# Kernel tuning notes

Measured on AMD Instinct MI355X. Metric: run time of the kernel, lower is better.

The kernel has to match this reference:

```python
import jax, jax.numpy as jnp
import numpy as np

# Graph configuration: G equal-sized graphs of N nodes each.
G, N, E, F = 64, 1024, 1_048_576, 256
RATIO, MULT = 0.5, 1.0
K = max(1, min(int(np.ceil(N * RATIO)), N))  # per-graph top-k = 512


def setup_inputs() -> dict:
    key = jax.random.key(0)
    k1, k2, k3, k4 = jax.random.split(key, 4)
    x = jax.random.normal(k1, (G * N, F), dtype=jnp.float32)
    # Edges constrained within a graph so per-graph pooling is meaningful.
    g = jax.random.randint(k2, (E,), 0, G)
    src = g * N + jax.random.randint(k3, (E,), 0, N)
    dst = g * N + jax.random.randint(k4, (E,), 0, N)
    edge_index = jnp.stack([src, dst]).astype(jnp.int32)  # [2, E]
    batch = jnp.repeat(jnp.arange(G, dtype=jnp.int32), N)  # [G*N]
    return {"x": x, "edge_index": edge_index, "batch": batch}


def reference(x, edge_index, batch):
    num_nodes = x.shape[0]
    # compute_score: out-degree via scatter-add of ones onto edge_index[0]
    degree = jnp.zeros(num_nodes, jnp.float32).at[edge_index[0]].add(1.0)
    score = degree  # min_score is None

    # Per-graph top-k. Graphs are equal-sized (N nodes), contiguous in batch
    # order, so the Python loop over graphs collapses to a batched top_k.
    _, topk_idx = jax.lax.top_k(score.reshape(G, N), K)  # [G, K]
    offsets = (jnp.arange(G, dtype=topk_idx.dtype) * N)[:, None]
    perm = (topk_idx + offsets).reshape(-1)  # [G*K] global node ids

    x_filtered = x[perm] * MULT
    batch_filtered = batch[perm]
    score_filtered = score[perm]

    # filter_edges_manual: keep edges whose both endpoints survive, remap ids.
    node_mask = jnp.zeros(num_nodes, bool).at[perm].set(True)
    edge_mask = node_mask[edge_index[1]] & node_mask[edge_index[0]]  # [E]
    node_map = jnp.full(num_nodes, -1, edge_index.dtype).at[perm].set(
        jnp.arange(perm.shape[0], dtype=edge_index.dtype))
    # Fixed-shape (jit-safe) variant of edge_index[:, edge_mask]: dropped
    # edges are marked -1; edge_mask identifies surviving edges.
    remapped_edge_index = jnp.where(edge_mask[None, :], node_map[edge_index], -1)

    return (x_filtered, remapped_edge_index, batch_filtered, perm,
            score_filtered, edge_mask)
```

## Files before the change

### kernel.cpp

```cpp
#include <hip/hip_runtime.h>


#define NG     64
#define NN     1024
#define NF     256
#define NK     512
#define HBLK   128
#define HWORDS 16384
#define NB2    256
#define EBLK   1024

__global__ void zero_kernel(int* __restrict__ p, int n) {
    int i = blockIdx.x * blockDim.x + threadIdx.x;
    if (i < n) p[i] = 0;
}

__global__ void degree_kernel(const int* __restrict__ ei_src,
                              int* __restrict__ deg, int E) {
    int e = blockIdx.x * blockDim.x + threadIdx.x;
    if (e < E) atomicAdd(&deg[ei_src[e]], 1);
}

__global__ __launch_bounds__(1024) void hist_kernel(
        const int* __restrict__ ei_src, unsigned int* __restrict__ hist_ws,
        int edges_per_blk) {
    __shared__ unsigned int h[HWORDS];
    const int tid = threadIdx.x;
    #pragma unroll
    for (int i = 0; i < HWORDS / 1024; ++i) h[i * 1024 + tid] = 0;
    __syncthreads();

    const int n4 = edges_per_blk >> 2;
    const int4* e4 = (const int4*)ei_src + (size_t)blockIdx.x * n4;
    for (int i = tid; i < n4; i += 1024) {
        const int4 v = e4[i];
        atomicAdd(&h[v.x >> 2], 1u << ((v.x & 3) << 3));
        atomicAdd(&h[v.y >> 2], 1u << ((v.y & 3) << 3));
        atomicAdd(&h[v.z >> 2], 1u << ((v.z & 3) << 3));
        atomicAdd(&h[v.w >> 2], 1u << ((v.w & 3) << 3));
    }
    __syncthreads();

    unsigned int* dst = hist_ws + (size_t)blockIdx.x * HWORDS;
    #pragma unroll
    for (int i = 0; i < HWORDS / 1024; ++i) dst[i * 1024 + tid] = h[i * 1024 + tid];
}

template <bool FUSED>
__global__ __launch_bounds__(1024) void rank_kernel(
        const unsigned int* __restrict__ hist_ws, const int* __restrict__ deg,
        int* __restrict__ node_map, float* __restrict__ out_perm,
        float* __restrict__ out_batch, float* __restrict__ out_score) {
    const int g = blockIdx.x, tid = threadIdx.x;
    const int wave = tid >> 6, lane = tid & 63;

    __shared__ unsigned int psum[4][256];
    __shared__ unsigned short whist[16][NB2];
    __shared__ int suf[NB2];

    ((unsigned int*)whist)[tid] = 0;
    ((unsigned int*)whist)[tid + 1024] = 0;

    int d;
    if (FUSED) {
        const int wl = tid & 255, grp = tid >> 8;
        const unsigned int* p =
            hist_ws + (size_t)(grp * 32) * HWORDS + (g * 256 + wl);
        unsigned int s = 0;
        #pragma unroll 8
        for (int b = 0; b < 32; ++b) s += p[(size_t)b * HWORDS];
        psum[grp][wl] = s;
        __syncthreads();
        const int w = tid >> 2, sh = (tid & 3) << 3;
        d = (int)((psum[0][w] >> sh) & 0xffu) + (int)((psum[1][w] >> sh) & 0xffu)
          + (int)((psum[2][w] >> sh) & 0xffu) + (int)((psum[3][w] >> sh) & 0xffu);
    } else {
        d = deg[g * NN + tid];
        __syncthreads();
    }
    const int b = d < NB2 ? d : (NB2 - 1);

    unsigned long long peers = ~0ull;
    #pragma unroll
    for (int k = 0; k < 8; ++k) {
        const bool bit = (b >> k) & 1;
        const unsigned long long m = __ballot(bit);
        peers &= bit ? m : ~m;
    }
    const unsigned long long lt = (1ull << lane) - 1ull;
    const int intra = __popcll(peers & lt);
    if (intra == 0)
        whist[wave][b] = (unsigned short)__popcll(peers);
    __syncthreads();

    if (tid < NB2) {
        int t = 0;
        #pragma unroll
        for (int w = 0; w < 16; ++w) t += whist[w][tid];
        suf[tid] = t;
    }
    __syncthreads();
    for (int off = 1; off < NB2; off <<= 1) {
        int v = 0;
        if (tid < NB2) v = suf[tid] + ((tid + off < NB2) ? suf[tid + off] : 0);
        __syncthreads();
        if (tid < NB2) suf[tid] = v;
        __syncthreads();
    }

    int cross = 0;
    for (int w = 0; w < 16; ++w) cross += (w < wave) ? whist[w][b] : 0;

    const int cnt_gt = (b < NB2 - 1) ? suf[b + 1] : 0;
    const int rank = cnt_gt + cross + intra;

    const int gid = g * NN + tid;
    const int nm = (rank < NK) ? (g * NK + rank) : -1;
    node_map[gid] = nm;
    if (nm >= 0) {
        out_perm[nm]  = (float)gid;
        out_batch[nm] = (float)g;
        out_score[nm] = (float)d;
    }
}

__global__ void out_kernel(const float* __restrict__ x,
                           const float* __restrict__ out_perm,
                           float* __restrict__ out_x,
                           const int* __restrict__ ei,
                           const int* __restrict__ node_map,
                           float* __restrict__ out_e,
                           float* __restrict__ out_mask, int E) {
    const int bid = blockIdx.x;
    if (bid < EBLK) {
        const int n4 = E >> 2;
        const int i = bid * 256 + threadIdx.x;
        if (i >= n4) return;
        const int4* e4 = (const int4*)ei;
        const int4 s = e4[i];
        const int4 t = e4[n4 + i];
        const int ms0 = node_map[s.x], ms1 = node_map[s.y];
        const int ms2 = node_map[s.z], ms3 = node_map[s.w];
        const int mt0 = node_map[t.x], mt1 = node_map[t.y];
        const int mt2 = node_map[t.z], mt3 = node_map[t.w];
        const bool k0 = (ms0 >= 0) & (mt0 >= 0);
        const bool k1 = (ms1 >= 0) & (mt1 >= 0);
        const bool k2 = (ms2 >= 0) & (mt2 >= 0);
        const bool k3 = (ms3 >= 0) & (mt3 >= 0);
        float4 es, et, mk;
        es.x = k0 ? (float)ms0 : -1.0f;  et.x = k0 ? (float)mt0 : -1.0f;
        es.y = k1 ? (float)ms1 : -1.0f;  et.y = k1 ? (float)mt1 : -1.0f;
        es.z = k2 ? (float)ms2 : -1.0f;  et.z = k2 ? (float)mt2 : -1.0f;
        es.w = k3 ? (float)ms3 : -1.0f;  et.w = k3 ? (float)mt3 : -1.0f;
        mk.x = k0 ? 1.0f : 0.0f;  mk.y = k1 ? 1.0f : 0.0f;
        mk.z = k2 ? 1.0f : 0.0f;  mk.w = k3 ? 1.0f : 0.0f;
        ((float4*)out_e)[i]      = es;
        ((float4*)out_e)[n4 + i] = et;
        ((float4*)out_mask)[i]   = mk;
    } else {
        const int flat = (bid - EBLK) * 256 + threadIdx.x;
        const int row  = flat >> 6;
        const int lane = flat & 63;
        if (row >= NG * NK) return;
        const int src = (int)out_perm[row];
        const float4* xs = (const float4*)(x + (size_t)src * NF);
        float4* xd = (float4*)(out_x + (size_t)row * NF);
        xd[lane] = xs[lane];
    }
}

extern "C" void kernel_launch(void* const* d_in, const int* in_sizes, int n_in,
                              void* d_out, int out_size, void* d_ws, size_t ws_size,
                              hipStream_t stream) {
    (void)n_in; (void)out_size;

    const float* x  = (const float*)d_in[0];
    const int*   ei = (const int*)d_in[1];
    const int E = in_sizes[1] / 2;
    const int num_nodes = in_sizes[2];

    float* out = (float*)d_out;
    size_t off = 0;
    float* out_x     = out + off; off += (size_t)NG * NK * NF;
    float* out_e     = out + off; off += 2 * (size_t)E;
    float* out_batch = out + off; off += (size_t)NG * NK;
    float* out_perm  = out + off; off += (size_t)NG * NK;
    float* out_score = out + off; off += (size_t)NG * NK;
    float* out_mask  = out + off;

    const int gather_blocks = (NG * NK * 64) / 256;
    const size_t hist_bytes = (size_t)HBLK * HWORDS * sizeof(unsigned int);
    const size_t need = hist_bytes + (size_t)num_nodes * sizeof(int);

    if (ws_size >= need) {
        unsigned int* hist_ws = (unsigned int*)d_ws;
        int* node_map = (int*)((char*)d_ws + hist_bytes);

        hist_kernel<<<HBLK, 1024, 0, stream>>>(ei, hist_ws, E / HBLK);
        rank_kernel<true><<<NG, 1024, 0, stream>>>(hist_ws, nullptr, node_map,
                                                   out_perm, out_batch, out_score);
        out_kernel<<<EBLK + gather_blocks, 256, 0, stream>>>(
            x, out_perm, out_x, ei, node_map, out_e, out_mask, E);
    } else {
        int* deg      = (int*)d_ws;
        int* node_map = deg + num_nodes;
        zero_kernel<<<(num_nodes + 255) / 256, 256, 0, stream>>>(deg, num_nodes);
        degree_kernel<<<(E + 255) / 256, 256, 0, stream>>>(ei, deg, E);
        rank_kernel<false><<<NG, 1024, 0, stream>>>(nullptr, deg, node_map,
                                                    out_perm, out_batch, out_score);
        out_kernel<<<EBLK + gather_blocks, 256, 0, stream>>>(
            x, out_perm, out_x, ei, node_map, out_e, out_mask, E);
    }
}
```

Baseline: 37.94 us.

## Split histogram reduction into a wide reduce kernel and double histogram blocks

Doubles the number of per-block edge histogram partials, so the histogram stage can spread over more compute units. Moves the cross-partial summation out of the 64-block rank kernel into a new 256-block reduce kernel that writes packed per-node degrees. The rank kernel then reads one packed word per four nodes. The cost is twice as much partial-histogram traffic written and read, plus one more kernel launch. It still relies on 8-bit packed counts not overflowing.

```diff
diff --git a/kernel.cpp b/kernel.cpp
--- a/kernel.cpp
+++ b/kernel.cpp
@@ -5,7 +5,7 @@
 #define NN     1024
 #define NF     256
 #define NK     512
-#define HBLK   128
+#define HBLK   256
 #define HWORDS 16384
 #define NB2    256
 #define EBLK   1024
@@ -46,37 +46,46 @@
     for (int i = 0; i < HWORDS / 1024; ++i) dst[i * 1024 + tid] = h[i * 1024 + tid];
 }
 
+__global__ __launch_bounds__(256) void reduce_kernel(
+        const unsigned int* __restrict__ hist_ws,
+        unsigned int* __restrict__ packed_deg) {
+    __shared__ unsigned int lsum[4][64];
+    const int t = threadIdx.x;
+    const int q = t >> 6, wl = t & 63;
+    const int w = blockIdx.x * 64 + wl;
+    const unsigned int* p = hist_ws + (size_t)(q * 64) * HWORDS + w;
+    unsigned int s = 0;
+    #pragma unroll 8
+    for (int j = 0; j < 64; ++j) s += p[(size_t)j * HWORDS];
+    lsum[q][wl] = s;
+    __syncthreads();
+    if (t < 64) {
+        packed_deg[blockIdx.x * 64 + t] =
+            lsum[0][t] + lsum[1][t] + lsum[2][t] + lsum[3][t];
+    }
+}
+
 template <bool FUSED>
 __global__ __launch_bounds__(1024) void rank_kernel(
-        const unsigned int* __restrict__ hist_ws, const int* __restrict__ deg,
+        const unsigned int* __restrict__ packed_deg, const int* __restrict__ deg,
         int* __restrict__ node_map, float* __restrict__ out_perm,
         float* __restrict__ out_batch, float* __restrict__ out_score) {
     const int g = blockIdx.x, tid = threadIdx.x;
     const int wave = tid >> 6, lane = tid & 63;
 
-    __shared__ unsigned int psum[4][256];
     __shared__ unsigned short whist[16][NB2];
     __shared__ int suf[NB2];
 
     ((unsigned int*)whist)[tid] = 0;
     ((unsigned int*)whist)[tid + 1024] = 0;
+    __syncthreads();
 
     int d;
     if (FUSED) {
-        const int wl = tid & 255, grp = tid >> 8;
-        const unsigned int* p =
-            hist_ws + (size_t)(grp * 32) * HWORDS + (g * 256 + wl);
-        unsigned int s = 0;
-        #pragma unroll 8
-        for (int b = 0; b < 32; ++b) s += p[(size_t)b * HWORDS];
-        psum[grp][wl] = s;
-        __syncthreads();
-        const int w = tid >> 2, sh = (tid & 3) << 3;
-        d = (int)((psum[0][w] >> sh) & 0xffu) + (int)((psum[1][w] >> sh) & 0xffu)
-          + (int)((psum[2][w] >> sh) & 0xffu) + (int)((psum[3][w] >> sh) & 0xffu);
+        const unsigned int w = packed_deg[g * 256 + (tid >> 2)];
+        d = (int)((w >> ((tid & 3) << 3)) & 0xffu);
     } else {
         d = deg[g * NN + tid];
-        __syncthreads();
     }
     const int b = d < NB2 ? d : (NB2 - 1);
 
@@ -190,14 +199,17 @@
 
     const int gather_blocks = (NG * NK * 64) / 256;
     const size_t hist_bytes = (size_t)HBLK * HWORDS * sizeof(unsigned int);
-    const size_t need = hist_bytes + (size_t)num_nodes * sizeof(int);
+    const size_t deg_bytes  = (size_t)HWORDS * sizeof(unsigned int);
+    const size_t need = hist_bytes + deg_bytes + (size_t)num_nodes * sizeof(int);
 
     if (ws_size >= need) {
-        unsigned int* hist_ws = (unsigned int*)d_ws;
-        int* node_map = (int*)((char*)d_ws + hist_bytes);
+        unsigned int* hist_ws    = (unsigned int*)d_ws;
+        unsigned int* packed_deg = hist_ws + (size_t)HBLK * HWORDS;
+        int* node_map = (int*)(packed_deg + HWORDS);
 
         hist_kernel<<<HBLK, 1024, 0, stream>>>(ei, hist_ws, E / HBLK);
-        rank_kernel<true><<<NG, 1024, 0, stream>>>(hist_ws, nullptr, node_map,
+        reduce_kernel<<<HWORDS / 64, 256, 0, stream>>>(hist_ws, packed_deg);
+        rank_kernel<true><<<NG, 1024, 0, stream>>>(packed_deg, nullptr, node_map,
                                                    out_perm, out_batch, out_score);
         out_kernel<<<EBLK + gather_blocks, 256, 0, stream>>>(
             x, out_perm, out_x, ei, node_map, out_e, out_mask, E);
```

New measurement: 40.87 us. 7.7% more time.

## Fuse histogram, rank and output stages into one persistent kernel with grid barriers

Applied to the files above, without the earlier changes.

Replaces the three-kernel pipeline (histogram, rank, output) with one persistent 256-block kernel that separates stages using software grid barriers built on agent-scope atomics. The degree reduction is split into its own parallel stage that writes packed degrees, so the rank stage only reads a small array. The intent is to remove two kernel launch gaps and use all blocks for the cross-histogram reduction. In exchange, correctness depends on all 256 blocks being co-resident, the barrier spin loop has a timeout that could silently break ordering, a memset is added per call, and only 64 blocks do useful work during the rank stage.

```diff
diff --git a/kernel.cpp b/kernel.cpp
--- a/kernel.cpp
+++ b/kernel.cpp
@@ -5,94 +5,218 @@
 #define NN     1024
 #define NF     256
 #define NK     512
-#define HBLK   128
+#define GRID   256
 #define HWORDS 16384
 #define NB2    256
-#define EBLK   1024
+
+__device__ __forceinline__ void grid_barrier(unsigned int* bar,
+                                             unsigned int target) {
+    __syncthreads();
+    if (threadIdx.x == 0) {
+        __threadfence();
+        const unsigned int old = __hip_atomic_fetch_add(
+            &bar[0], 1u, __ATOMIC_ACQ_REL, __HIP_MEMORY_SCOPE_AGENT);
+        if (old == GRID - 1) {
+            __hip_atomic_store(&bar[0], 0u, __ATOMIC_RELAXED,
+                               __HIP_MEMORY_SCOPE_AGENT);
+            __hip_atomic_store(&bar[1], target, __ATOMIC_RELEASE,
+                               __HIP_MEMORY_SCOPE_AGENT);
+        } else {
+            long spins = 0;
+            while (__hip_atomic_load(&bar[1], __ATOMIC_ACQUIRE,
+                                     __HIP_MEMORY_SCOPE_AGENT) < target) {
+                __builtin_amdgcn_s_sleep(8);
+                if (++spins > (1L << 19)) break;
+            }
+        }
+        __threadfence();
+    }
+    __syncthreads();
+}
+
+__global__ __launch_bounds__(1024, 4) void fused_kernel(
+        const float* __restrict__ x, const int* __restrict__ ei,
+        unsigned int* __restrict__ hist_ws, unsigned int* __restrict__ packed_deg,
+        int* __restrict__ node_map, unsigned int* __restrict__ bar,
+        float* __restrict__ out_x, float* __restrict__ out_e,
+        float* __restrict__ out_batch, float* __restrict__ out_perm,
+        float* __restrict__ out_score, float* __restrict__ out_mask, int E) {
+    __shared__ unsigned int lds[HWORDS];
+    const int b = blockIdx.x, tid = threadIdx.x;
+    const int n4 = E >> 2;
+    const int per_blk4 = n4 / GRID;
+    const int4* e4 = (const int4*)ei;
+
+    #pragma unroll
+    for (int i = 0; i < HWORDS / 1024; ++i) lds[i * 1024 + tid] = 0;
+    __syncthreads();
+    for (int i = tid; i < per_blk4; i += 1024) {
+        const int4 v = e4[b * per_blk4 + i];
+        atomicAdd(&lds[v.x >> 2], 1u << ((v.x & 3) << 3));
+        atomicAdd(&lds[v.y >> 2], 1u << ((v.y & 3) << 3));
+        atomicAdd(&lds[v.z >> 2], 1u << ((v.z & 3) << 3));
+        atomicAdd(&lds[v.w >> 2], 1u << ((v.w & 3) << 3));
+    }
+    __syncthreads();
+    {
+        unsigned int* dst = hist_ws + (size_t)b * HWORDS;
+        #pragma unroll
+        for (int i = 0; i < HWORDS / 1024; ++i)
+            dst[i * 1024 + tid] = lds[i * 1024 + tid];
+    }
+
+    grid_barrier(bar, 1);
+
+    {
+        const int q = tid >> 6, wl = tid & 63;
+        const unsigned int* p =
+            hist_ws + (size_t)(q * 16) * HWORDS + (b * 64 + wl);
+        unsigned int s = 0;
+        #pragma unroll
+        for (int j = 0; j < 16; ++j) s += p[(size_t)j * HWORDS];
+        lds[q * 64 + wl] = s;
+        __syncthreads();
+        if (tid < 64) {
+            unsigned int t = 0;
+            #pragma unroll
+            for (int q2 = 0; q2 < 16; ++q2) t += lds[q2 * 64 + tid];
+            packed_deg[b * 64 + tid] = t;
+        }
+    }
+
+    grid_barrier(bar, 2);
+
+    if (b < NG) {
+        const int g = b;
+        const int wave = tid >> 6, lane = tid & 63;
+        unsigned short* whist = (unsigned short*)lds;
+        int* suf = (int*)(lds + 2048);
+
+        ((unsigned int*)whist)[tid] = 0;
+        ((unsigned int*)whist)[tid + 1024] = 0;
+        __syncthreads();
+
+        const unsigned int w = packed_deg[g * 256 + (tid >> 2)];
+        const int d = (int)((w >> ((tid & 3) << 3)) & 0xffu);
+        const int bk = d < NB2 ? d : (NB2 - 1);
+
+        unsigned long long peers = ~0ull;
+        #pragma unroll
+        for (int k = 0; k < 8; ++k) {
+            const bool bit = (bk >> k) & 1;
+            const unsigned long long m = __ballot(bit);
+            peers &= bit ? m : ~m;
+        }
+        const unsigned long long lt = (1ull << lane) - 1ull;
+        const int intra = __popcll(peers & lt);
+        if (intra == 0)
+            whist[wave * NB2 + bk] = (unsigned short)__popcll(peers);
+        __syncthreads();
+
+        if (tid < NB2) {
+            int t = 0;
+            #pragma unroll
+            for (int wv = 0; wv < 16; ++wv) t += whist[wv * NB2 + tid];
+            suf[tid] = t;
+        }
+        __syncthreads();
+        for (int off = 1; off < NB2; off <<= 1) {
+            int v = 0;
+            if (tid < NB2)
+                v = suf[tid] + ((tid + off < NB2) ? suf[tid + off] : 0);
+            __syncthreads();
+            if (tid < NB2) suf[tid] = v;
+            __syncthreads();
+        }
+
+        int cross = 0;
+        for (int wv = 0; wv < 16; ++wv)
+            cross += (wv < wave) ? whist[wv * NB2 + bk] : 0;
+
+        const int cnt_gt = (bk < NB2 - 1) ? suf[bk + 1] : 0;
+        const int rank = cnt_gt + cross + intra;
+
+        const int gid = g * NN + tid;
+        const int nm = (rank < NK) ? (g * NK + rank) : -1;
+        node_map[gid] = nm;
+        if (nm >= 0) {
+            out_perm[nm]  = (float)gid;
+            out_batch[nm] = (float)g;
+            out_score[nm] = (float)d;
+        }
+    }
+
+    grid_barrier(bar, 3);
+
+    for (int i = tid; i < per_blk4; i += 1024) {
+        const int idx = b * per_blk4 + i;
+        const int4 s = e4[idx];
+        const int4 t = e4[n4 + idx];
+        const int ms0 = node_map[s.x], ms1 = node_map[s.y];
+        const int ms2 = node_map[s.z], ms3 = node_map[s.w];
+        const int mt0 = node_map[t.x], mt1 = node_map[t.y];
+        const int mt2 = node_map[t.z], mt3 = node_map[t.w];
+        const bool k0 = (ms0 >= 0) & (mt0 >= 0);
+        const bool k1 = (ms1 >= 0) & (mt1 >= 0);
+        const bool k2 = (ms2 >= 0) & (mt2 >= 0);
+        const bool k3 = (ms3 >= 0) & (mt3 >= 0);
+        float4 es, et, mk;
+        es.x = k0 ? (float)ms0 : -1.0f;  et.x = k0 ? (float)mt0 : -1.0f;
+        es.y = k1 ? (float)ms1 : -1.0f;  et.y = k1 ? (float)mt1 : -1.0f;
+        es.z = k2 ? (float)ms2 : -1.0f;  et.z = k2 ? (float)mt2 : -1.0f;
+        es.w = k3 ? (float)ms3 : -1.0f;  et.w = k3 ? (float)mt3 : -1.0f;
+        mk.x = k0 ? 1.0f : 0.0f;  mk.y = k1 ? 1.0f : 0.0f;
+        mk.z = k2 ? 1.0f : 0.0f;  mk.w = k3 ? 1.0f : 0.0f;
+        ((float4*)out_e)[idx]      = es;
+        ((float4*)out_e)[n4 + idx] = et;
+        ((float4*)out_mask)[idx]   = mk;
+    }
+
+    {
+        const int wave = tid >> 6, lane = tid & 63;
+        #pragma unroll
+        for (int r = 0; r < 8; ++r) {
+            const int row = b * 128 + r * 16 + wave;
+            const int src = (int)out_perm[row];
+            ((float4*)(out_x + (size_t)row * NF))[lane] =
+                ((const float4*)(x + (size_t)src * NF))[lane];
+        }
+    }
+}
 
 __global__ void zero_kernel(int* __restrict__ p, int n) {
     int i = blockIdx.x * blockDim.x + threadIdx.x;
     if (i < n) p[i] = 0;
 }
-
 __global__ void degree_kernel(const int* __restrict__ ei_src,
                               int* __restrict__ deg, int E) {
     int e = blockIdx.x * blockDim.x + threadIdx.x;
     if (e < E) atomicAdd(&deg[ei_src[e]], 1);
 }
-
-__global__ __launch_bounds__(1024) void hist_kernel(
-        const int* __restrict__ ei_src, unsigned int* __restrict__ hist_ws,
-        int edges_per_blk) {
-    __shared__ unsigned int h[HWORDS];
-    const int tid = threadIdx.x;
-    #pragma unroll
-    for (int i = 0; i < HWORDS / 1024; ++i) h[i * 1024 + tid] = 0;
-    __syncthreads();
-
-    const int n4 = edges_per_blk >> 2;
-    const int4* e4 = (const int4*)ei_src + (size_t)blockIdx.x * n4;
-    for (int i = tid; i < n4; i += 1024) {
-        const int4 v = e4[i];
-        atomicAdd(&h[v.x >> 2], 1u << ((v.x & 3) << 3));
-        atomicAdd(&h[v.y >> 2], 1u << ((v.y & 3) << 3));
-        atomicAdd(&h[v.z >> 2], 1u << ((v.z & 3) << 3));
-        atomicAdd(&h[v.w >> 2], 1u << ((v.w & 3) << 3));
-    }
-    __syncthreads();
-
-    unsigned int* dst = hist_ws + (size_t)blockIdx.x * HWORDS;
-    #pragma unroll
-    for (int i = 0; i < HWORDS / 1024; ++i) dst[i * 1024 + tid] = h[i * 1024 + tid];
-}
-
-template <bool FUSED>
-__global__ __launch_bounds__(1024) void rank_kernel(
-        const unsigned int* __restrict__ hist_ws, const int* __restrict__ deg,
-        int* __restrict__ node_map, float* __restrict__ out_perm,
-        float* __restrict__ out_batch, float* __restrict__ out_score) {
+__global__ __launch_bounds__(1024) void rank_fb_kernel(
+        const int* __restrict__ deg, int* __restrict__ node_map,
+        float* __restrict__ out_perm, float* __restrict__ out_batch,
+        float* __restrict__ out_score) {
     const int g = blockIdx.x, tid = threadIdx.x;
     const int wave = tid >> 6, lane = tid & 63;
-
-    __shared__ unsigned int psum[4][256];
     __shared__ unsigned short whist[16][NB2];
     __shared__ int suf[NB2];
-
     ((unsigned int*)whist)[tid] = 0;
     ((unsigned int*)whist)[tid + 1024] = 0;
-
-    int d;
-    if (FUSED) {
-        const int wl = tid & 255, grp = tid >> 8;
-        const unsigned int* p =
-            hist_ws + (size_t)(grp * 32) * HWORDS + (g * 256 + wl);
-        unsigned int s = 0;
-        #pragma unroll 8
-        for (int b = 0; b < 32; ++b) s += p[(size_t)b * HWORDS];
-        psum[grp][wl] = s;
-        __syncthreads();
-        const int w = tid >> 2, sh = (tid & 3) << 3;
-        d = (int)((psum[0][w] >> sh) & 0xffu) + (int)((psum[1][w] >> sh) & 0xffu)
-          + (int)((psum[2][w] >> sh) & 0xffu) + (int)((psum[3][w] >> sh) & 0xffu);
-    } else {
-        d = deg[g * NN + tid];
-        __syncthreads();
-    }
-    const int b = d < NB2 ? d : (NB2 - 1);
-
+    __syncthreads();
+    const int d = deg[g * NN + tid];
+    const int bk = d < NB2 ? d : (NB2 - 1);
     unsigned long long peers = ~0ull;
     #pragma unroll
     for (int k = 0; k < 8; ++k) {
-        const bool bit = (b >> k) & 1;
+        const bool bit = (bk >> k) & 1;
         const unsigned long long m = __ballot(bit);
         peers &= bit ? m : ~m;
     }
     const unsigned long long lt = (1ull << lane) - 1ull;
     const int intra = __popcll(peers & lt);
-    if (intra == 0)
-        whist[wave][b] = (unsigned short)__popcll(peers);
-    __syncthreads();
-
+    if (intra == 0) whist[wave][bk] = (unsigned short)__popcll(peers);
+    __syncthreads();
     if (tid < NB2) {
         int t = 0;
         #pragma unroll
@@ -107,13 +231,9 @@
         if (tid < NB2) suf[tid] = v;
         __syncthreads();
     }
-
     int cross = 0;
-    for (int w = 0; w < 16; ++w) cross += (w < wave) ? whist[w][b] : 0;
-
-    const int cnt_gt = (b < NB2 - 1) ? suf[b + 1] : 0;
-    const int rank = cnt_gt + cross + intra;
-
+    for (int w = 0; w < 16; ++w) cross += (w < wave) ? whist[w][bk] : 0;
+    const int rank = ((bk < NB2 - 1) ? suf[bk + 1] : 0) + cross + intra;
     const int gid = g * NN + tid;
     const int nm = (rank < NK) ? (g * NK + rank) : -1;
     node_map[gid] = nm;
@@ -123,16 +243,15 @@
         out_score[nm] = (float)d;
     }
 }
-
-__global__ void out_kernel(const float* __restrict__ x,
-                           const float* __restrict__ out_perm,
-                           float* __restrict__ out_x,
-                           const int* __restrict__ ei,
-                           const int* __restrict__ node_map,
-                           float* __restrict__ out_e,
-                           float* __restrict__ out_mask, int E) {
+__global__ void out_fb_kernel(const float* __restrict__ x,
+                              const float* __restrict__ out_perm,
+                              float* __restrict__ out_x,
+                              const int* __restrict__ ei,
+                              const int* __restrict__ node_map,
+                              float* __restrict__ out_e,
+                              float* __restrict__ out_mask, int E) {
     const int bid = blockIdx.x;
-    if (bid < EBLK) {
+    if (bid < 1024) {
         const int n4 = E >> 2;
         const int i = bid * 256 + threadIdx.x;
         if (i >= n4) return;
@@ -158,14 +277,13 @@
         ((float4*)out_e)[n4 + i] = et;
         ((float4*)out_mask)[i]   = mk;
     } else {
-        const int flat = (bid - EBLK) * 256 + threadIdx.x;
+        const int flat = (bid - 1024) * 256 + threadIdx.x;
         const int row  = flat >> 6;
         const int lane = flat & 63;
         if (row >= NG * NK) return;
         const int src = (int)out_perm[row];
-        const float4* xs = (const float4*)(x + (size_t)src * NF);
-        float4* xd = (float4*)(out_x + (size_t)row * NF);
-        xd[lane] = xs[lane];
+        ((float4*)(out_x + (size_t)row * NF))[lane] =
+            ((const float4*)(x + (size_t)src * NF))[lane];
     }
 }
 
@@ -188,27 +306,29 @@
     float* out_score = out + off; off += (size_t)NG * NK;
     float* out_mask  = out + off;
 
-    const int gather_blocks = (NG * NK * 64) / 256;
-    const size_t hist_bytes = (size_t)HBLK * HWORDS * sizeof(unsigned int);
-    const size_t need = hist_bytes + (size_t)num_nodes * sizeof(int);
-
-    if (ws_size >= need) {
-        unsigned int* hist_ws = (unsigned int*)d_ws;
-        int* node_map = (int*)((char*)d_ws + hist_bytes);
-
-        hist_kernel<<<HBLK, 1024, 0, stream>>>(ei, hist_ws, E / HBLK);
-        rank_kernel<true><<<NG, 1024, 0, stream>>>(hist_ws, nullptr, node_map,
-                                                   out_perm, out_batch, out_score);
-        out_kernel<<<EBLK + gather_blocks, 256, 0, stream>>>(
-            x, out_perm, out_x, ei, node_map, out_e, out_mask, E);
+    const size_t hist_bytes = (size_t)GRID * HWORDS * sizeof(unsigned int);
+    const size_t deg_bytes  = (size_t)HWORDS * sizeof(unsigned int);
+    const size_t map_bytes  = (size_t)num_nodes * sizeof(int);
+    const size_t need = hist_bytes + deg_bytes + map_bytes + 16;
+
+    if (ws_size >= need && E == (1 << 20) && num_nodes == NG * NN) {
+        unsigned int* hist_ws    = (unsigned int*)d_ws;
+        unsigned int* packed_deg = hist_ws + (size_t)GRID * HWORDS;
+        int* node_map            = (int*)(packed_deg + HWORDS);
+        unsigned int* bar        = (unsigned int*)(node_map + num_nodes);
+
+        hipMemsetAsync(bar, 0, 16, stream);
+        fused_kernel<<<GRID, 1024, 0, stream>>>(
+            x, ei, hist_ws, packed_deg, node_map, bar,
+            out_x, out_e, out_batch, out_perm, out_score, out_mask, E);
     } else {
         int* deg      = (int*)d_ws;
         int* node_map = deg + num_nodes;
         zero_kernel<<<(num_nodes + 255) / 256, 256, 0, stream>>>(deg, num_nodes);
         degree_kernel<<<(E + 255) / 256, 256, 0, stream>>>(ei, deg, E);
-        rank_kernel<false><<<NG, 1024, 0, stream>>>(nullptr, deg, node_map,
-                                                    out_perm, out_batch, out_score);
-        out_kernel<<<EBLK + gather_blocks, 256, 0, stream>>>(
+        rank_fb_kernel<<<NG, 1024, 0, stream>>>(deg, node_map, out_perm,
+                                                out_batch, out_score);
+        out_fb_kernel<<<1024 + (NG * NK * 64) / 256, 256, 0, stream>>>(
             x, out_perm, out_x, ei, node_map, out_e, out_mask, E);
     }
 }
```

After: 138.2 us. +264.2%, slower.
